# Optimization experiments

Measured on AMD Instinct MI355X. Metric: run time of the kernel, lower is better.

## Reference

```python
import jax, jax.numpy as jnp
import numpy as np

BN_EPS = 1e-5


def setup_inputs() -> dict:
    key = jax.random.key(0)
    ks = jax.random.split(key, 8)
    B, N, S, D1, D2 = 8, 8192, 2048, 128, 256
    C0, C1, C2 = D1 + D2, 256, 128
    return {
        "xyz_sa": jax.random.normal(ks[0], (B, 3, N), dtype=jnp.float32),
        "xyz_now": jax.random.normal(ks[1], (B, 3, S), dtype=jnp.float32),
        "points_sa": jax.random.normal(ks[2], (B, D1, N), dtype=jnp.float32),
        "points_now": jax.random.normal(ks[3], (B, D2, S), dtype=jnp.float32),
        "W0": jax.random.normal(ks[4], (C1, C0), dtype=jnp.float32) * (1.0 / np.sqrt(C0)),
        "b0": jax.random.normal(ks[5], (C1,), dtype=jnp.float32) * 0.01,
        "g0": jnp.ones((C1,), dtype=jnp.float32),
        "be0": jnp.zeros((C1,), dtype=jnp.float32),
        "W1": jax.random.normal(ks[6], (C2, C1), dtype=jnp.float32) * (1.0 / np.sqrt(C1)),
        "b1": jax.random.normal(ks[7], (C2,), dtype=jnp.float32) * 0.01,
        "g1": jnp.ones((C2,), dtype=jnp.float32),
        "be1": jnp.zeros((C2,), dtype=jnp.float32),
        "k": 3,
    }


def _conv_bn_relu(x, W, b, g, beta):
    # 1x1 Conv2d over [B, C, N, 1] == channel matmul; BN2d training-mode
    # batch stats over (B, N); then ReLU.
    y = jnp.einsum("oc,bcn->bon", W, x) + b[None, :, None]
    mean = jnp.mean(y, axis=(0, 2), keepdims=True)
    var = jnp.var(y, axis=(0, 2), keepdims=True)  # biased var, as BN uses
    yn = (y - mean) * jax.lax.rsqrt(var + BN_EPS)
    return jax.nn.relu(yn * g[None, :, None] + beta[None, :, None])


def reference(xyz_sa, xyz_now, points_sa, points_now,
              W0, b0, g0, be0, W1, b1, g1, be1, k):
    xs = xyz_sa.transpose(0, 2, 1)      # [B, N, 3]
    xn = xyz_now.transpose(0, 2, 1)     # [B, S, 3]
    pn = points_now.transpose(0, 2, 1)  # [B, S, D2]
    # squared pairwise distances [B, N, S]
    d = (jnp.sum(xs * xs, axis=-1)[:, :, None]
         - 2.0 * jnp.einsum("bnc,bsc->bns", xs, xn)
         + jnp.sum(xn * xn, axis=-1)[:, None, :])
    # k smallest distances (ascending), same as sort + slice [:, :, :k]
    neg_d, idx = jax.lax.top_k(-d, k)           # [B, N, k]
    dists = -neg_d
    dist_recip = 1.0 / (dists + 1e-8)
    weight = dist_recip / jnp.sum(dist_recip, axis=-1, keepdims=True)  # [B,N,k]
    gathered = jax.vmap(lambda p, i: p[i])(pn, idx)   # [B, N, k, D2]
    interp = jnp.sum(gathered * weight[..., None], axis=2)  # [B, N, D2]
    feat = jnp.concatenate([points_sa.transpose(0, 2, 1), interp], axis=-1)
    x = feat.transpose(0, 2, 1)  # [B, D1+D2, N]
    x = _conv_bn_relu(x, W0, b0, g0, be0)
    x = _conv_bn_relu(x, W1, b1, g1, be1)
    return x  # [B, mlp[-1], N]
```

## Files before the change

kernel.cpp:

```cpp
#include <hip/hip_runtime.h>

#define B_ 8
#define N_ 8192
#define S_ 2048
#define D1_ 128
#define D2_ 256
#define C0_ 384
#define C1_ 256
#define C2_ 128
#define BN_EPS 1e-5f

typedef unsigned long long ull;
typedef unsigned short u16;
typedef __bf16 bf16x8 __attribute__((ext_vector_type(8)));
typedef float f32x4 __attribute__((ext_vector_type(4)));
typedef short short8_ __attribute__((ext_vector_type(8)));

__device__ __forceinline__ u16 f2bf(float x) {
  unsigned int u = __float_as_uint(x);
  unsigned int r = u + 0x7fffu + ((u >> 16) & 1u);
  return (u16)(r >> 16);
}
__device__ __forceinline__ float bf2f(u16 h) {
  return __uint_as_float(((unsigned int)h) << 16);
}

__device__ __forceinline__ void gld16(const void* g, void* l) {
  __builtin_amdgcn_global_load_lds(
      (const __attribute__((address_space(1))) void*)g,
      (__attribute__((address_space(3))) void*)l,
      16, 0, 0);
}

__device__ __forceinline__ void insf(float d, int i,
    float& D0, int& I0, float& D1, int& I1, float& D2, int& I2) {
  bool c2 = d < D2, c1 = d < D1, c0 = d < D0;
  D2 = c1 ? D1 : (c2 ? d : D2);  I2 = c1 ? I1 : (c2 ? i : I2);
  D1 = c0 ? D0 : (c1 ? d : D1);  I1 = c0 ? I0 : (c1 ? i : I1);
  D0 = c0 ? d : D0;              I0 = c0 ? i : I0;
}

__global__ void cvtW_kernel(const float* __restrict__ src, u16* __restrict__ dst,
                            int O, int K)
{
  int i = blockIdx.x * blockDim.x + threadIdx.x;
  if (i < O * K) {
    int o = i / K, kk = i - o * K;
    dst[(((size_t)(kk >> 5) * O + o) << 5) + (kk & 31)] = f2bf(src[i]);
  }
}

__global__ __launch_bounds__(256) void transpose_kernel(
    const float* __restrict__ in, float* __restrict__ out)
{
  __shared__ float tile[32][33];
  const int b  = blockIdx.z;
  const int s0 = blockIdx.x * 32;
  const int d0 = blockIdx.y * 32;
  const int tx = threadIdx.x & 31, ty = threadIdx.x >> 5;

  const float* inb = in + ((size_t)b * D2_ + d0) * S_ + s0;
  #pragma unroll
  for (int r = 0; r < 4; ++r) {
    int d = r * 8 + ty;
    tile[d][tx] = inb[(size_t)d * S_ + tx];
  }
  __syncthreads();
  float* outb = out + ((size_t)b * S_ + s0) * D2_ + d0;
  #pragma unroll
  for (int r = 0; r < 4; ++r) {
    int s = r * 8 + ty;
    outb[(size_t)s * D2_ + tx] = tile[tx][s];
  }
}

__global__ __launch_bounds__(256) void psaT_kernel(
    const float* __restrict__ in, u16* __restrict__ xcat)
{
  __shared__ float tile[32][33];
  const int b  = blockIdx.z;
  const int n0 = blockIdx.x * 32;
  const int d0 = blockIdx.y * 32;
  const int tx = threadIdx.x & 31, ty = threadIdx.x >> 5;

  const float* inb = in + ((size_t)b * D1_ + d0) * N_ + n0;
  #pragma unroll
  for (int r = 0; r < 4; ++r) {
    int d = r * 8 + ty;
    tile[d][tx] = inb[(size_t)d * N_ + tx];
  }
  __syncthreads();
  u16* outb = xcat + (((size_t)b * 12 + (d0 >> 5)) * N_ + n0) * 32;
  #pragma unroll
  for (int r = 0; r < 4; ++r) {
    int n = r * 8 + ty;
    outb[(size_t)n * 32 + tx] = f2bf(tile[tx][n]);
  }
}

__global__ __launch_bounds__(256) void knn_interp_kernel(
    const float* __restrict__ xyz_sa, const float* __restrict__ xyz_now,
    const float* __restrict__ pnT, u16* __restrict__ xcat)
{
  __shared__ float4 sp[1024];
  __shared__ int   s_idx[32][3];
  __shared__ float s_w[32][3];

  const int b  = blockIdx.y;
  const int n0 = blockIdx.x * 32;

  const int qg = threadIdx.x >> 4;
  const int t  = threadIdx.x & 15;
  const int nb = n0 + qg * 2;

  const float* xq = xyz_sa + (size_t)b * 3 * N_;
  float qx[2], qy[2], qz[2], qq[2];
  #pragma unroll
  for (int w = 0; w < 2; ++w) {
    int n = nb + w;
    qx[w] = xq[n]; qy[w] = xq[N_ + n]; qz[w] = xq[2 * N_ + n];
    qq[w] = qx[w] * qx[w] + qy[w] * qy[w] + qz[w] * qz[w];
  }

  float D0[2], D1[2], D2[2];
  int   I0[2], I1[2], I2[2];
  #pragma unroll
  for (int w = 0; w < 2; ++w) {
    D0[w] = 3.4e38f; D1[w] = 3.4e38f; D2[w] = 3.4e38f;
    I0[w] = 0; I1[w] = 0; I2[w] = 0;
  }

  const float* xb = xyz_now + (size_t)b * 3 * S_;
  for (int chunk = 0; chunk < 2; ++chunk) {
    const int sbase = chunk << 10;
    for (int i = threadIdx.x; i < 1024; i += 256) {
      int sg = sbase + i;
      float px = xb[sg], py = xb[S_ + sg], pz = xb[2 * S_ + sg];
      sp[i] = make_float4(-2.f * px, -2.f * py, -2.f * pz,
                          px * px + py * py + pz * pz);
    }
    __syncthreads();

    #pragma unroll 4
    for (int it = 0; it < 64; ++it) {
      int sl = (it << 4) | t;
      float4 p = sp[sl];
      int sg = sbase + sl;
      #pragma unroll
      for (int w = 0; w < 2; ++w) {
        float d = fmaf(p.x, qx[w], fmaf(p.y, qy[w], fmaf(p.z, qz[w], p.w)));
        insf(d, sg, D0[w], I0[w], D1[w], I1[w], D2[w], I2[w]);
      }
    }
    __syncthreads();
  }

  #pragma unroll
  for (int m = 1; m <= 8; m <<= 1) {
    #pragma unroll
    for (int w = 0; w < 2; ++w) {
      float e0 = __shfl_xor(D0[w], m), e1 = __shfl_xor(D1[w], m), e2 = __shfl_xor(D2[w], m);
      int   j0 = __shfl_xor(I0[w], m), j1 = __shfl_xor(I1[w], m), j2 = __shfl_xor(I2[w], m);
      insf(e0, j0, D0[w], I0[w], D1[w], I1[w], D2[w], I2[w]);
      insf(e1, j1, D0[w], I0[w], D1[w], I1[w], D2[w], I2[w]);
      insf(e2, j2, D0[w], I0[w], D1[w], I1[w], D2[w], I2[w]);
    }
  }

  if (t == 0) {
    #pragma unroll
    for (int w = 0; w < 2; ++w) {
      float d0 = D0[w] + qq[w];
      float d1 = D1[w] + qq[w];
      float d2 = D2[w] + qq[w];
      float r0 = 1.0f / (d0 + 1e-8f);
      float r1 = 1.0f / (d1 + 1e-8f);
      float r2 = 1.0f / (d2 + 1e-8f);
      float rs = 1.0f / (r0 + r1 + r2);
      int qi = qg * 2 + w;
      s_idx[qi][0] = I0[w];
      s_idx[qi][1] = I1[w];
      s_idx[qi][2] = I2[w];
      s_w[qi][0] = r0 * rs; s_w[qi][1] = r1 * rs; s_w[qi][2] = r2 * rs;
    }
  }
  __syncthreads();

  const int wave = threadIdx.x >> 6;
  const int lane = threadIdx.x & 63;
  const int c8 = lane >> 3;
  const int k4 = (lane & 7) * 4;
  const float* pb = pnT + (size_t)b * S_ * D2_ + c8 * 32 + k4;
  u16* ob = xcat + (((size_t)b * 12 + 4 + c8) * N_ + n0) * 32 + k4;
  #pragma unroll 2
  for (int i = 0; i < 8; ++i) {
    const int qi = wave * 8 + i;
    const int j0 = s_idx[qi][0], j1 = s_idx[qi][1], j2 = s_idx[qi][2];
    const float w0 = s_w[qi][0], w1 = s_w[qi][1], w2 = s_w[qi][2];
    float4 f0 = *(const float4*)(pb + (size_t)j0 * D2_);
    float4 f1 = *(const float4*)(pb + (size_t)j1 * D2_);
    float4 f2 = *(const float4*)(pb + (size_t)j2 * D2_);
    float rx = w0 * f0.x + w1 * f1.x + w2 * f2.x;
    float ry = w0 * f0.y + w1 * f1.y + w2 * f2.y;
    float rz = w0 * f0.z + w1 * f1.z + w2 * f2.z;
    float rw = w0 * f0.w + w1 * f1.w + w2 * f2.w;
    unsigned int lo = (unsigned int)f2bf(rx) | ((unsigned int)f2bf(ry) << 16);
    unsigned int hi = (unsigned int)f2bf(rz) | ((unsigned int)f2bf(rw) << 16);
    *(uint2*)(ob + (size_t)qi * 32) = make_uint2(lo, hi);
  }
}

union SMg {
  struct { u16 As[2][4096]; u16 Bs[2][4096]; } p;
  u16 stage[128][136];
};

__global__ __launch_bounds__(256) void gemm1_mfma_kernel(
    const u16* __restrict__ xcat, const u16* __restrict__ W0b,
    const float* __restrict__ b0, u16* __restrict__ y0b, float* __restrict__ partials)
{
  __shared__ SMg sm;

  const int bz = blockIdx.z;
  const int n0 = blockIdx.x * 128;
  const int o0 = blockIdx.y * 128;
  const int tid = threadIdx.x;
  const int wid = tid >> 6, lane = tid & 63;
  const int wo = wid & 1, wn = wid >> 1;
  const int m = lane & 15, g = lane >> 4;

  f32x4 acc[4][4];
  #pragma unroll
  for (int i = 0; i < 4; ++i)
    #pragma unroll
    for (int j = 0; j < 4; ++j) acc[i][j] = (f32x4){0.f, 0.f, 0.f, 0.f};

  auto STAGE = [&](int buf, int c) {
    const u16* asrc = W0b  + ((size_t)c * C1_ + o0) * 32;
    const u16* bsrc = xcat + (((size_t)bz * 12 + c) * N_ + n0) * 32;
    #pragma unroll
    for (int i2 = 0; i2 < 2; ++i2) {
      const int i = wid * 2 + i2;
      gld16(asrc + i * 512 + lane * 8, &sm.p.As[buf][i * 512]);
      gld16(bsrc + i * 512 + lane * 8, &sm.p.Bs[buf][i * 512]);
    }
  };

  STAGE(0, 0);
  __syncthreads();

  for (int kt = 0; kt < 12; ++kt) {
    const int cur = kt & 1;
    if (kt < 11) STAGE(cur ^ 1, kt + 1);

    bf16x8 af[4], bfv[4];
    #pragma unroll
    for (int f = 0; f < 4; ++f)
      af[f] = __builtin_bit_cast(bf16x8,
          *(const short8_*)&sm.p.As[cur][(wo * 64 + f * 16 + m) * 32 + g * 8]);
    #pragma unroll
    for (int f = 0; f < 4; ++f)
      bfv[f] = __builtin_bit_cast(bf16x8,
          *(const short8_*)&sm.p.Bs[cur][(wn * 64 + f * 16 + m) * 32 + g * 8]);
    #pragma unroll
    for (int i = 0; i < 4; ++i)
      #pragma unroll
      for (int j = 0; j < 4; ++j)
        acc[i][j] = __builtin_amdgcn_mfma_f32_16x16x32_bf16(af[i], bfv[j], acc[i][j], 0, 0, 0);

    __syncthreads();
  }

  const int slot = (blockIdx.x * 8 + bz) * 2 + wn;
  float* prow = partials + (size_t)slot * 512;

  #pragma unroll
  for (int of = 0; of < 4; ++of) {
    const int ol = wo * 64 + of * 16 + g * 4;
    const int ob = o0 + ol;
    float bias[4], s1[4], s2[4];
    #pragma unroll
    for (int r = 0; r < 4; ++r) { bias[r] = b0[ob + r]; s1[r] = 0.f; s2[r] = 0.f; }
    #pragma unroll
    for (int nf = 0; nf < 4; ++nf) {
      const int nl = wn * 64 + nf * 16 + m;
      float y[4];
      #pragma unroll
      for (int r = 0; r < 4; ++r) {
        y[r] = acc[of][nf][r] + bias[r];
        s1[r] += y[r]; s2[r] += y[r] * y[r];
      }
      unsigned int lo = (unsigned int)f2bf(y[0]) | ((unsigned int)f2bf(y[1]) << 16);
      unsigned int hi = (unsigned int)f2bf(y[2]) | ((unsigned int)f2bf(y[3]) << 16);
      *(uint2*)&sm.stage[nl][ol] = make_uint2(lo, hi);
    }
    #pragma unroll
    for (int mk = 1; mk < 16; mk <<= 1)
      #pragma unroll
      for (int r = 0; r < 4; ++r) {
        s1[r] += __shfl_xor(s1[r], mk);
        s2[r] += __shfl_xor(s2[r], mk);
      }
    if (m == 0) {
      *(float4*)(prow + ob)        = make_float4(s1[0], s1[1], s1[2], s1[3]);
      *(float4*)(prow + 256 + ob)  = make_float4(s2[0], s2[1], s2[2], s2[3]);
    }
  }
  __syncthreads();
  {
    const int rrow = tid >> 4;
    const int col  = (tid & 15) * 8;
    const int c    = (o0 + col) >> 5;
    const int ko   = (o0 + col) & 31;
    u16* dst = y0b + (((size_t)bz * 8 + c) * N_ + n0) * 32 + ko;
    #pragma unroll
    for (int pass = 0; pass < 8; ++pass) {
      const int r = pass * 16 + rrow;
      *(uint4*)(dst + (size_t)r * 32) = *(const uint4*)&sm.stage[r][col];
    }
  }
}

__global__ __launch_bounds__(256) void reduce_coef_kernel(
    const float* __restrict__ partials, int R, int C,
    const float* __restrict__ g, const float* __restrict__ be,
    float* __restrict__ coef)
{
  const int ch = blockIdx.x;
  const int tid = threadIdx.x;
  float s = 0.f, q = 0.f;
  #pragma unroll
  for (int k = 0; k < 4; ++k) {
    const float* row = partials + (size_t)(tid + k * 256) * R;
    s += row[ch];
    q += row[C + ch];
  }
  #pragma unroll
  for (int mk = 1; mk < 64; mk <<= 1) { s += __shfl_xor(s, mk); q += __shfl_xor(q, mk); }
  __shared__ float ls[4], lq[4];
  const int wid = tid >> 6;
  if ((tid & 63) == 0) { ls[wid] = s; lq[wid] = q; }
  __syncthreads();
  if (tid == 0) {
    s = ls[0] + ls[1] + ls[2] + ls[3];
    q = lq[0] + lq[1] + lq[2] + lq[3];
    const float invM = 1.0f / 65536.0f;
    float mean = s * invM;
    float var  = q * invM - mean * mean;
    float a = g[ch] / sqrtf(var + BN_EPS);
    float c = be[ch] - mean * a;
    coef[ch] = a;
    coef[C + ch] = c;
  }
}

__global__ __launch_bounds__(256) void bn0relu_kernel(
    const u16* __restrict__ y0b, const float* __restrict__ coef, u16* __restrict__ y0r)
{
  __shared__ float cfa[C1_], cfc[C1_];
  cfa[threadIdx.x] = coef[threadIdx.x];
  cfc[threadIdx.x] = coef[C1_ + threadIdx.x];
  __syncthreads();
  const size_t total8 = (size_t)B_ * N_ * C1_ / 8;
  const size_t stride = (size_t)gridDim.x * blockDim.x;
  for (size_t i = (size_t)blockIdx.x * blockDim.x + threadIdx.x; i < total8; i += stride) {
    uint4 v = *(const uint4*)(y0b + i * 8);
    const int ch = (int)(((i >> 15) & 7) * 32 + ((i * 8) & 31));
    float f0 = fmaxf(0.f, fmaf(bf2f((u16)(v.x & 0xffff)), cfa[ch + 0], cfc[ch + 0]));
    float f1 = fmaxf(0.f, fmaf(bf2f((u16)(v.x >> 16)),    cfa[ch + 1], cfc[ch + 1]));
    float f2 = fmaxf(0.f, fmaf(bf2f((u16)(v.y & 0xffff)), cfa[ch + 2], cfc[ch + 2]));
    float f3 = fmaxf(0.f, fmaf(bf2f((u16)(v.y >> 16)),    cfa[ch + 3], cfc[ch + 3]));
    float f4 = fmaxf(0.f, fmaf(bf2f((u16)(v.z & 0xffff)), cfa[ch + 4], cfc[ch + 4]));
    float f5 = fmaxf(0.f, fmaf(bf2f((u16)(v.z >> 16)),    cfa[ch + 5], cfc[ch + 5]));
    float f6 = fmaxf(0.f, fmaf(bf2f((u16)(v.w & 0xffff)), cfa[ch + 6], cfc[ch + 6]));
    float f7 = fmaxf(0.f, fmaf(bf2f((u16)(v.w >> 16)),    cfa[ch + 7], cfc[ch + 7]));
    uint4 o;
    o.x = (unsigned int)f2bf(f0) | ((unsigned int)f2bf(f1) << 16);
    o.y = (unsigned int)f2bf(f2) | ((unsigned int)f2bf(f3) << 16);
    o.z = (unsigned int)f2bf(f4) | ((unsigned int)f2bf(f5) << 16);
    o.w = (unsigned int)f2bf(f6) | ((unsigned int)f2bf(f7) << 16);
    *(uint4*)(y0r + i * 8) = o;
  }
}

__global__ __launch_bounds__(256) void gemm2_mfma_kernel(
    const u16* __restrict__ y0r, const u16* __restrict__ W1b,
    const float* __restrict__ b1, u16* __restrict__ y1b, float* __restrict__ partials)
{
  __shared__ SMg sm;

  const int bz = blockIdx.z;
  const int n0 = blockIdx.x * 128;
  const int tid = threadIdx.x;
  const int wid = tid >> 6, lane = tid & 63;
  const int wo = wid & 1, wn = wid >> 1;
  const int m = lane & 15, g = lane >> 4;

  f32x4 acc[4][4];
  #pragma unroll
  for (int i = 0; i < 4; ++i)
    #pragma unroll
    for (int j = 0; j < 4; ++j) acc[i][j] = (f32x4){0.f, 0.f, 0.f, 0.f};

  auto STAGE = [&](int buf, int c) {
    const u16* asrc = W1b + ((size_t)c * C2_) * 32;
    const u16* bsrc = y0r + (((size_t)bz * 8 + c) * N_ + n0) * 32;
    #pragma unroll
    for (int i2 = 0; i2 < 2; ++i2) {
      const int i = wid * 2 + i2;
      gld16(asrc + i * 512 + lane * 8, &sm.p.As[buf][i * 512]);
      gld16(bsrc + i * 512 + lane * 8, &sm.p.Bs[buf][i * 512]);
    }
  };

  STAGE(0, 0);
  __syncthreads();

  for (int kt = 0; kt < 8; ++kt) {
    const int cur = kt & 1;
    if (kt < 7) STAGE(cur ^ 1, kt + 1);

    bf16x8 af[4], bfv[4];
    #pragma unroll
    for (int f = 0; f < 4; ++f)
      af[f] = __builtin_bit_cast(bf16x8,
          *(const short8_*)&sm.p.As[cur][(wo * 64 + f * 16 + m) * 32 + g * 8]);
    #pragma unroll
    for (int f = 0; f < 4; ++f)
      bfv[f] = __builtin_bit_cast(bf16x8,
          *(const short8_*)&sm.p.Bs[cur][(wn * 64 + f * 16 + m) * 32 + g * 8]);
    #pragma unroll
    for (int i = 0; i < 4; ++i)
      #pragma unroll
      for (int j = 0; j < 4; ++j)
        acc[i][j] = __builtin_amdgcn_mfma_f32_16x16x32_bf16(af[i], bfv[j], acc[i][j], 0, 0, 0);

    __syncthreads();
  }

  const int slot = (blockIdx.x * 8 + bz) * 2 + wn;
  float* prow = partials + (size_t)slot * 256;

  #pragma unroll
  for (int of = 0; of < 4; ++of) {
    const int pb = wo * 64 + of * 16 + g * 4;
    float bias[4], s1[4], s2[4];
    #pragma unroll
    for (int r = 0; r < 4; ++r) { bias[r] = b1[pb + r]; s1[r] = 0.f; s2[r] = 0.f; }
    #pragma unroll
    for (int nf = 0; nf < 4; ++nf) {
      const int nl = wn * 64 + nf * 16 + m;
      #pragma unroll
      for (int r = 0; r < 4; ++r) {
        float y = acc[of][nf][r] + bias[r];
        s1[r] += y; s2[r] += y * y;
        sm.stage[pb + r][nl] = f2bf(y);
      }
    }
    #pragma unroll
    for (int mk = 1; mk < 16; mk <<= 1)
      #pragma unroll
      for (int r = 0; r < 4; ++r) {
        s1[r] += __shfl_xor(s1[r], mk);
        s2[r] += __shfl_xor(s2[r], mk);
      }
    if (m == 0) {
      *(float4*)(prow + pb)        = make_float4(s1[0], s1[1], s1[2], s1[3]);
      *(float4*)(prow + 128 + pb)  = make_float4(s2[0], s2[1], s2[2], s2[3]);
    }
  }
  __syncthreads();
  {
    #pragma unroll
    for (int pass = 0; pass < 8; ++pass) {
      const int idx = pass * 256 + tid;
      const int p = idx >> 4;
      const int c8 = (idx & 15) * 8;
      uint4 v = *(const uint4*)&sm.stage[p][c8];
      *(uint4*)(y1b + ((size_t)bz * C2_ + p) * N_ + n0 + c8) = v;
    }
  }
}

__global__ __launch_bounds__(256) void final_kernel(
    const u16* __restrict__ y1b, const float* __restrict__ cf, float* __restrict__ out)
{
  const size_t total4 = (size_t)B_ * C2_ * N_ / 4;
  const size_t stride = (size_t)gridDim.x * blockDim.x;
  for (size_t f = (size_t)blockIdx.x * blockDim.x + threadIdx.x; f < total4; f += stride) {
    size_t base = f * 4;
    int p = (int)((base >> 13) & (C2_ - 1));
    float a = cf[p], c = cf[C2_ + p];
    uint2 v = *(const uint2*)(y1b + base);
    float4 r;
    r.x = fmaxf(0.0f, fmaf(bf2f((u16)(v.x & 0xffff)), a, c));
    r.y = fmaxf(0.0f, fmaf(bf2f((u16)(v.x >> 16)),    a, c));
    r.z = fmaxf(0.0f, fmaf(bf2f((u16)(v.y & 0xffff)), a, c));
    r.w = fmaxf(0.0f, fmaf(bf2f((u16)(v.y >> 16)),    a, c));
    *(float4*)(out + base) = r;
  }
}

extern "C" void kernel_launch(void* const* d_in, const int* in_sizes, int n_in,
                              void* d_out, int out_size, void* d_ws, size_t ws_size,
                              hipStream_t stream)
{
  const float* xyz_sa     = (const float*)d_in[0];
  const float* xyz_now    = (const float*)d_in[1];
  const float* points_sa  = (const float*)d_in[2];
  const float* points_now = (const float*)d_in[3];
  const float* W0  = (const float*)d_in[4];
  const float* b0  = (const float*)d_in[5];
  const float* g0  = (const float*)d_in[6];
  const float* be0 = (const float*)d_in[7];
  const float* W1  = (const float*)d_in[8];
  const float* b1  = (const float*)d_in[9];
  const float* g1  = (const float*)d_in[10];
  const float* be1 = (const float*)d_in[11];

  const size_t MB = 1048576ull;
  char* base = (char*)d_ws;
  u16*   xcat  = (u16*)(base + 0);
  u16*   y0r   = (u16*)(base + 0);
  float* pnT   = (float*)(base + 48 * MB);
  u16*   y1b   = (u16*)(base + 48 * MB);
  u16*   y0b   = (u16*)(base + 64 * MB);
  u16*   W0b   = (u16*)(base + 96 * MB);
  u16*   W1b   = (u16*)(base + 96 * MB + 512 * 1024);
  float* coef  = (float*)(base + 97 * MB);
  float* part1 = (float*)(base + 98 * MB);
  float* part2 = (float*)(base + 100 * MB);
  float* out   = (float*)d_out;

  hipLaunchKernelGGL(cvtW_kernel, dim3((C1_ * C0_ + 255) / 256), dim3(256), 0, stream,
                     W0, W0b, C1_, C0_);
  hipLaunchKernelGGL(cvtW_kernel, dim3((C2_ * C1_ + 255) / 256), dim3(256), 0, stream,
                     W1, W1b, C2_, C1_);
  hipLaunchKernelGGL(transpose_kernel, dim3(S_ / 32, D2_ / 32, B_), dim3(256), 0, stream,
                     points_now, pnT);
  hipLaunchKernelGGL(psaT_kernel, dim3(N_ / 32, D1_ / 32, B_), dim3(256), 0, stream,
                     points_sa, xcat);
  hipLaunchKernelGGL(knn_interp_kernel, dim3(N_ / 32, B_), dim3(256), 0, stream,
                     xyz_sa, xyz_now, pnT, xcat);
  hipLaunchKernelGGL(gemm1_mfma_kernel, dim3(N_ / 128, 2, B_), dim3(256), 0, stream,
                     xcat, W0b, b0, y0b, part1);
  hipLaunchKernelGGL(reduce_coef_kernel, dim3(C1_), dim3(256), 0, stream,
                     part1, 512, C1_, g0, be0, coef);
  hipLaunchKernelGGL(bn0relu_kernel, dim3(2048), dim3(256), 0, stream,
                     y0b, coef, y0r);
  hipLaunchKernelGGL(gemm2_mfma_kernel, dim3(N_ / 128, 1, B_), dim3(256), 0, stream,
                     y0r, W1b, b1, y1b, part2);
  hipLaunchKernelGGL(reduce_coef_kernel, dim3(C2_), dim3(256), 0, stream,
                     part2, 256, C2_, g1, be1, coef + 512);
  hipLaunchKernelGGL(final_kernel, dim3(2048), dim3(256), 0, stream,
                     y1b, coef + 512, out);
}
```

Measured before the change: 179.3 us.

## Split KNN into value-only med3 top-3 pass and thresholded index pass

The nearest-neighbour search first finds the third-smallest distance per query using cheap fmed3/fmin value-only insertion, with no index tracking. A second pass recomputes distances and performs the full index-tracking insertion only for candidates at or below that threshold. This cuts the per-candidate select work in the hot loop. In exchange it computes every distance twice, reloads the point tile into shared memory, and adds a divergent branch.

Measured after the change: 178.4 us. No clear change (-0.5%).

```diff
diff --git a/kernel.cpp b/kernel.cpp
--- a/kernel.cpp
+++ b/kernel.cpp
@@ -40,6 +40,12 @@
   D0 = c0 ? d : D0;              I0 = c0 ? i : I0;
 }
 
+__device__ __forceinline__ void insv(float d, float& D0, float& D1, float& D2) {
+  D2 = __builtin_amdgcn_fmed3f(D1, D2, d);
+  D1 = __builtin_amdgcn_fmed3f(D0, D1, d);
+  D0 = fminf(D0, d);
+}
+
 __global__ void cvtW_kernel(const float* __restrict__ src, u16* __restrict__ dst,
                             int O, int K)
 {
@@ -114,23 +120,19 @@
   const int nb = n0 + qg * 2;
 
   const float* xq = xyz_sa + (size_t)b * 3 * N_;
-  float qx[2], qy[2], qz[2], qq[2];
+  float qx[2], qy[2], qz[2];
   #pragma unroll
   for (int w = 0; w < 2; ++w) {
     int n = nb + w;
     qx[w] = xq[n]; qy[w] = xq[N_ + n]; qz[w] = xq[2 * N_ + n];
-    qq[w] = qx[w] * qx[w] + qy[w] * qy[w] + qz[w] * qz[w];
-  }
+  }
+
+  const float* xb = xyz_now + (size_t)b * 3 * S_;
 
   float D0[2], D1[2], D2[2];
-  int   I0[2], I1[2], I2[2];
-  #pragma unroll
-  for (int w = 0; w < 2; ++w) {
-    D0[w] = 3.4e38f; D1[w] = 3.4e38f; D2[w] = 3.4e38f;
-    I0[w] = 0; I1[w] = 0; I2[w] = 0;
-  }
-
-  const float* xb = xyz_now + (size_t)b * 3 * S_;
+  #pragma unroll
+  for (int w = 0; w < 2; ++w) { D0[w] = 3.4e38f; D1[w] = 3.4e38f; D2[w] = 3.4e38f; }
+
   for (int chunk = 0; chunk < 2; ++chunk) {
     const int sbase = chunk << 10;
     for (int i = threadIdx.x; i < 1024; i += 256) {
@@ -145,11 +147,10 @@
     for (int it = 0; it < 64; ++it) {
       int sl = (it << 4) | t;
       float4 p = sp[sl];
-      int sg = sbase + sl;
       #pragma unroll
       for (int w = 0; w < 2; ++w) {
         float d = fmaf(p.x, qx[w], fmaf(p.y, qy[w], fmaf(p.z, qz[w], p.w)));
-        insf(d, sg, D0[w], I0[w], D1[w], I1[w], D2[w], I2[w]);
+        insv(d, D0[w], D1[w], D2[w]);
       }
     }
     __syncthreads();
@@ -160,27 +161,75 @@
     #pragma unroll
     for (int w = 0; w < 2; ++w) {
       float e0 = __shfl_xor(D0[w], m), e1 = __shfl_xor(D1[w], m), e2 = __shfl_xor(D2[w], m);
-      int   j0 = __shfl_xor(I0[w], m), j1 = __shfl_xor(I1[w], m), j2 = __shfl_xor(I2[w], m);
-      insf(e0, j0, D0[w], I0[w], D1[w], I1[w], D2[w], I2[w]);
-      insf(e1, j1, D0[w], I0[w], D1[w], I1[w], D2[w], I2[w]);
-      insf(e2, j2, D0[w], I0[w], D1[w], I1[w], D2[w], I2[w]);
+      insv(e0, D0[w], D1[w], D2[w]);
+      insv(e1, D0[w], D1[w], D2[w]);
+      insv(e2, D0[w], D1[w], D2[w]);
+    }
+  }
+  const float thr0 = D2[0], thr1 = D2[1];
+
+  float bD0[2], bD1[2], bD2[2];
+  int   bI0[2], bI1[2], bI2[2];
+  #pragma unroll
+  for (int w = 0; w < 2; ++w) {
+    bD0[w] = 3.4e38f; bD1[w] = 3.4e38f; bD2[w] = 3.4e38f;
+    bI0[w] = 0; bI1[w] = 0; bI2[w] = 0;
+  }
+
+  for (int chunk = 0; chunk < 2; ++chunk) {
+    const int sbase = chunk << 10;
+    for (int i = threadIdx.x; i < 1024; i += 256) {
+      int sg = sbase + i;
+      float px = xb[sg], py = xb[S_ + sg], pz = xb[2 * S_ + sg];
+      sp[i] = make_float4(-2.f * px, -2.f * py, -2.f * pz,
+                          px * px + py * py + pz * pz);
+    }
+    __syncthreads();
+
+    #pragma unroll 2
+    for (int it = 0; it < 64; ++it) {
+      int sl = (it << 4) | t;
+      float4 p = sp[sl];
+      int sg = sbase + sl;
+      float da = fmaf(p.x, qx[0], fmaf(p.y, qy[0], fmaf(p.z, qz[0], p.w)));
+      float db = fmaf(p.x, qx[1], fmaf(p.y, qy[1], fmaf(p.z, qz[1], p.w)));
+      bool h0 = da <= thr0;
+      bool h1 = db <= thr1;
+      if (h0 | h1) {
+        if (h0) insf(da, sg, bD0[0], bI0[0], bD1[0], bI1[0], bD2[0], bI2[0]);
+        if (h1) insf(db, sg, bD0[1], bI0[1], bD1[1], bI1[1], bD2[1], bI2[1]);
+      }
+    }
+    __syncthreads();
+  }
+
+  #pragma unroll
+  for (int m = 1; m <= 8; m <<= 1) {
+    #pragma unroll
+    for (int w = 0; w < 2; ++w) {
+      float e0 = __shfl_xor(bD0[w], m), e1 = __shfl_xor(bD1[w], m), e2 = __shfl_xor(bD2[w], m);
+      int   j0 = __shfl_xor(bI0[w], m), j1 = __shfl_xor(bI1[w], m), j2 = __shfl_xor(bI2[w], m);
+      insf(e0, j0, bD0[w], bI0[w], bD1[w], bI1[w], bD2[w], bI2[w]);
+      insf(e1, j1, bD0[w], bI0[w], bD1[w], bI1[w], bD2[w], bI2[w]);
+      insf(e2, j2, bD0[w], bI0[w], bD1[w], bI1[w], bD2[w], bI2[w]);
     }
   }
 
   if (t == 0) {
     #pragma unroll
     for (int w = 0; w < 2; ++w) {
-      float d0 = D0[w] + qq[w];
-      float d1 = D1[w] + qq[w];
-      float d2 = D2[w] + qq[w];
+      float qq = qx[w] * qx[w] + qy[w] * qy[w] + qz[w] * qz[w];
+      float d0 = bD0[w] + qq;
+      float d1 = bD1[w] + qq;
+      float d2 = bD2[w] + qq;
       float r0 = 1.0f / (d0 + 1e-8f);
       float r1 = 1.0f / (d1 + 1e-8f);
       float r2 = 1.0f / (d2 + 1e-8f);
       float rs = 1.0f / (r0 + r1 + r2);
       int qi = qg * 2 + w;
-      s_idx[qi][0] = I0[w];
-      s_idx[qi][1] = I1[w];
-      s_idx[qi][2] = I2[w];
+      s_idx[qi][0] = bI0[w];
+      s_idx[qi][1] = bI1[w];
+      s_idx[qi][2] = bI2[w];
       s_w[qi][0] = r0 * rs; s_w[qi][1] = r1 * rs; s_w[qi][2] = r2 * rs;
     }
   }
```

## Fuse BN0 normalize+ReLU into GEMM2 operand staging via register prefetch

Applied to the files above, without the earlier changes.

Removes the standalone bn0relu pass that read y0b and wrote y0r. GEMM2 now loads raw y0b tiles into registers, applies the per-channel BN affine and ReLU, converts to bf16, and writes the result into shared memory for the MFMA loop. The next tile's global load is issued before the current tile's MFMAs so its latency overlaps compute. This saves one full read and write of the 32 MB intermediate plus a kernel launch, at the cost of more registers and VALU work inside the GEMM loop.

Result: faster. 173.1 us (-3.4%).

```diff
diff --git a/kernel.cpp b/kernel.cpp
--- a/kernel.cpp
+++ b/kernel.cpp
@@ -354,40 +354,13 @@
   }
 }
 
-__global__ __launch_bounds__(256) void bn0relu_kernel(
-    const u16* __restrict__ y0b, const float* __restrict__ coef, u16* __restrict__ y0r)
-{
+__global__ __launch_bounds__(256) void gemm2_mfma_kernel(
+    const u16* __restrict__ y0b, const float* __restrict__ coef,
+    const u16* __restrict__ W1b, const float* __restrict__ b1,
+    u16* __restrict__ y1b, float* __restrict__ partials)
+{
+  __shared__ SMg sm;
   __shared__ float cfa[C1_], cfc[C1_];
-  cfa[threadIdx.x] = coef[threadIdx.x];
-  cfc[threadIdx.x] = coef[C1_ + threadIdx.x];
-  __syncthreads();
-  const size_t total8 = (size_t)B_ * N_ * C1_ / 8;
-  const size_t stride = (size_t)gridDim.x * blockDim.x;
-  for (size_t i = (size_t)blockIdx.x * blockDim.x + threadIdx.x; i < total8; i += stride) {
-    uint4 v = *(const uint4*)(y0b + i * 8);
-    const int ch = (int)(((i >> 15) & 7) * 32 + ((i * 8) & 31));
-    float f0 = fmaxf(0.f, fmaf(bf2f((u16)(v.x & 0xffff)), cfa[ch + 0], cfc[ch + 0]));
-    float f1 = fmaxf(0.f, fmaf(bf2f((u16)(v.x >> 16)),    cfa[ch + 1], cfc[ch + 1]));
-    float f2 = fmaxf(0.f, fmaf(bf2f((u16)(v.y & 0xffff)), cfa[ch + 2], cfc[ch + 2]));
-    float f3 = fmaxf(0.f, fmaf(bf2f((u16)(v.y >> 16)),    cfa[ch + 3], cfc[ch + 3]));
-    float f4 = fmaxf(0.f, fmaf(bf2f((u16)(v.z & 0xffff)), cfa[ch + 4], cfc[ch + 4]));
-    float f5 = fmaxf(0.f, fmaf(bf2f((u16)(v.z >> 16)),    cfa[ch + 5], cfc[ch + 5]));
-    float f6 = fmaxf(0.f, fmaf(bf2f((u16)(v.w & 0xffff)), cfa[ch + 6], cfc[ch + 6]));
-    float f7 = fmaxf(0.f, fmaf(bf2f((u16)(v.w >> 16)),    cfa[ch + 7], cfc[ch + 7]));
-    uint4 o;
-    o.x = (unsigned int)f2bf(f0) | ((unsigned int)f2bf(f1) << 16);
-    o.y = (unsigned int)f2bf(f2) | ((unsigned int)f2bf(f3) << 16);
-    o.z = (unsigned int)f2bf(f4) | ((unsigned int)f2bf(f5) << 16);
-    o.w = (unsigned int)f2bf(f6) | ((unsigned int)f2bf(f7) << 16);
-    *(uint4*)(y0r + i * 8) = o;
-  }
-}
-
-__global__ __launch_bounds__(256) void gemm2_mfma_kernel(
-    const u16* __restrict__ y0r, const u16* __restrict__ W1b,
-    const float* __restrict__ b1, u16* __restrict__ y1b, float* __restrict__ partials)
-{
-  __shared__ SMg sm;
 
   const int bz = blockIdx.z;
   const int n0 = blockIdx.x * 128;
@@ -396,29 +369,65 @@
   const int wo = wid & 1, wn = wid >> 1;
   const int m = lane & 15, g = lane >> 4;
 
+  cfa[tid] = coef[tid];
+  cfc[tid] = coef[C1_ + tid];
+
   f32x4 acc[4][4];
   #pragma unroll
   for (int i = 0; i < 4; ++i)
     #pragma unroll
     for (int j = 0; j < 4; ++j) acc[i][j] = (f32x4){0.f, 0.f, 0.f, 0.f};
 
-  auto STAGE = [&](int buf, int c) {
+  auto STAGE_A = [&](int buf, int c) {
     const u16* asrc = W1b + ((size_t)c * C2_) * 32;
-    const u16* bsrc = y0r + (((size_t)bz * 8 + c) * N_ + n0) * 32;
     #pragma unroll
     for (int i2 = 0; i2 < 2; ++i2) {
       const int i = wid * 2 + i2;
       gld16(asrc + i * 512 + lane * 8, &sm.p.As[buf][i * 512]);
-      gld16(bsrc + i * 512 + lane * 8, &sm.p.Bs[buf][i * 512]);
     }
   };
 
-  STAGE(0, 0);
+  uint4 rb[2];
+  auto BLOAD = [&](int c) {
+    const u16* bsrc = y0b + (((size_t)bz * 8 + c) * N_ + n0) * 32 + tid * 8;
+    rb[0] = *(const uint4*)bsrc;
+    rb[1] = *(const uint4*)(bsrc + 2048);
+  };
+  auto BWRITE = [&](int buf, int c) {
+    const int ch = c * 32 + (tid & 3) * 8;
+    float a0 = cfa[ch + 0], a1 = cfa[ch + 1], a2 = cfa[ch + 2], a3 = cfa[ch + 3];
+    float a4 = cfa[ch + 4], a5 = cfa[ch + 5], a6 = cfa[ch + 6], a7 = cfa[ch + 7];
+    float c0 = cfc[ch + 0], c1 = cfc[ch + 1], c2 = cfc[ch + 2], c3 = cfc[ch + 3];
+    float c4 = cfc[ch + 4], c5 = cfc[ch + 5], c6 = cfc[ch + 6], c7 = cfc[ch + 7];
+    #pragma unroll
+    for (int h = 0; h < 2; ++h) {
+      uint4 v = rb[h];
+      float f0 = fmaxf(0.f, fmaf(bf2f((u16)(v.x & 0xffff)), a0, c0));
+      float f1 = fmaxf(0.f, fmaf(bf2f((u16)(v.x >> 16)),    a1, c1));
+      float f2 = fmaxf(0.f, fmaf(bf2f((u16)(v.y & 0xffff)), a2, c2));
+      float f3 = fmaxf(0.f, fmaf(bf2f((u16)(v.y >> 16)),    a3, c3));
+      float f4 = fmaxf(0.f, fmaf(bf2f((u16)(v.z & 0xffff)), a4, c4));
+      float f5 = fmaxf(0.f, fmaf(bf2f((u16)(v.z >> 16)),    a5, c5));
+      float f6 = fmaxf(0.f, fmaf(bf2f((u16)(v.w & 0xffff)), a6, c6));
+      float f7 = fmaxf(0.f, fmaf(bf2f((u16)(v.w >> 16)),    a7, c7));
+      uint4 o;
+      o.x = (unsigned int)f2bf(f0) | ((unsigned int)f2bf(f1) << 16);
+      o.y = (unsigned int)f2bf(f2) | ((unsigned int)f2bf(f3) << 16);
+      o.z = (unsigned int)f2bf(f4) | ((unsigned int)f2bf(f5) << 16);
+      o.w = (unsigned int)f2bf(f6) | ((unsigned int)f2bf(f7) << 16);
+      *(uint4*)&sm.p.Bs[buf][h * 2048 + tid * 8] = o;
+    }
+  };
+
+  BLOAD(0);
+  STAGE_A(0, 0);
+  __syncthreads();
+  BWRITE(0, 0);
   __syncthreads();
 
   for (int kt = 0; kt < 8; ++kt) {
     const int cur = kt & 1;
-    if (kt < 7) STAGE(cur ^ 1, kt + 1);
+    if (kt < 7) { STAGE_A(cur ^ 1, kt + 1); BLOAD(kt + 1); }
 
     bf16x8 af[4], bfv[4];
     #pragma unroll
@@ -435,6 +444,7 @@
       for (int j = 0; j < 4; ++j)
         acc[i][j] = __builtin_amdgcn_mfma_f32_16x16x32_bf16(af[i], bfv[j], acc[i][j], 0, 0, 0);
 
+    if (kt < 7) BWRITE(cur ^ 1, kt + 1);
     __syncthreads();
   }
 
@@ -521,7 +531,6 @@
   const size_t MB = 1048576ull;
   char* base = (char*)d_ws;
   u16*   xcat  = (u16*)(base + 0);
-  u16*   y0r   = (u16*)(base + 0);
   float* pnT   = (float*)(base + 48 * MB);
   u16*   y1b   = (u16*)(base + 48 * MB);
   u16*   y0b   = (u16*)(base + 64 * MB);
@@ -546,10 +555,8 @@
                      xcat, W0b, b0, y0b, part1);
   hipLaunchKernelGGL(reduce_coef_kernel, dim3(C1_), dim3(256), 0, stream,
                      part1, 512, C1_, g0, be0, coef);
-  hipLaunchKernelGGL(bn0relu_kernel, dim3(2048), dim3(256), 0, stream,
-                     y0b, coef, y0r);
   hipLaunchKernelGGL(gemm2_mfma_kernel, dim3(N_ / 128, 1, B_), dim3(256), 0, stream,
-                     y0r, W1b, b1, y1b, part2);
+                     y0b, coef, W1b, b1, y1b, part2);
   hipLaunchKernelGGL(reduce_coef_kernel, dim3(C2_), dim3(256), 0, stream,
                      part2, 256, C2_, g1, be1, coef + 512);
   hipLaunchKernelGGL(final_kernel, dim3(2048), dim3(256), 0, stream,
```
